# Performance work log

Hardware: AMD Instinct MI355X
Metric: run time of the kernel (lower is better)

## Reference

```python
import jax, jax.numpy as jnp
import numpy as np

B, DIM_Z, N_SAMPLES = 256, 64, 32
LOG_2PI = float(np.log(2.0 * np.pi))
VAR_EPS = 0.0001


def log_pdf(mean, logvar, zs):
    # elementwise Gaussian log-density (per dim), matching torch log_pdf
    return -0.5 * LOG_2PI - 0.5 * logvar - (zs - mean) ** 2 / (2.0 * jnp.exp(logvar) + VAR_EPS)


def setup_inputs() -> dict:
    key = jax.random.key(0)
    k1, k2, k3, k4, k5 = jax.random.split(key, 5)
    return {
        "prior_mean": jax.random.normal(k1, (B, DIM_Z), dtype=jnp.float32),
        "prior_logvar": jax.random.normal(k2, (B, DIM_Z), dtype=jnp.float32),
        "post_mean": jax.random.normal(k3, (B, DIM_Z), dtype=jnp.float32),
        "post_logvar": jax.random.normal(k4, (B, DIM_Z), dtype=jnp.float32),
        "eps": jax.random.normal(k5, (B, DIM_Z, N_SAMPLES), dtype=jnp.float32),
    }


def reference(prior_mean, prior_logvar, post_mean, post_logvar, eps):
    batch_size = post_mean.shape[0]
    # reparameterized samples from each posterior: [B, D, S]
    zs = post_mean[:, :, None] + eps * jnp.exp(0.5 * post_logvar)[:, :, None]
    # log p_prior_j(z_{j,d,s}): [B, D, S]
    logp_priors_zs = log_pdf(prior_mean[:, :, None], prior_logvar[:, :, None], zs)
    # log p_post_i(z_{j,d,s}): [B(i), B(j), D, S] -- the big broadcast intermediate
    logp_posts_zs = log_pdf(post_mean[:, None, :, None], post_logvar[:, None, :, None], zs[None])
    # max-stabilized log-mean-exp over posteriors i == logsumexp - log(B)
    logp_agg_post_zs = jax.scipy.special.logsumexp(logp_posts_zs, axis=0) - jnp.log(
        jnp.asarray(batch_size, dtype=logp_posts_zs.dtype)
    )  # [B(j), D, S]
    density_gaps = logp_agg_post_zs - logp_priors_zs  # [B, D, S]
    kl = density_gaps.mean(axis=0)  # [D, S]
    kl = kl.sum(axis=0).mean(axis=-1)  # scalar
    return kl
```

## Files before the change

### kernel.cpp

```cpp
#include <hip/hip_runtime.h>
#include <math.h>

#define BATCH 256
#define DIMZ  64
#define NSAMP 32
#define JB    32

__global__ __launch_bounds__(256) void lpo_tbl_kernel(
    const float* __restrict__ post_mean,
    const float* __restrict__ post_logvar,
    float* __restrict__ tblA,
    float* __restrict__ tblB,
    float* __restrict__ tblC)
{
    constexpr float LOG_2PI = 1.8378770664093453f;
    constexpr float VAR_EPS = 1e-4f;
    constexpr float LOG2E   = 1.4426950408889634f;

    const int d = blockIdx.x;
    const int i = threadIdx.x;

    const float m   = post_mean[i * DIMZ + d];
    const float lv  = post_logvar[i * DIMZ + d];
    const float den = 2.0f * __expf(lv) + VAR_EPS;
    const float C   = LOG2E / den;
    const float B   = 2.0f * m * C;
    const float A   = LOG2E * (-0.5f * LOG_2PI - 0.5f * lv) - m * m * C;

    tblA[d * BATCH + i] = A;
    tblB[d * BATCH + i] = B;
    tblC[d * BATCH + i] = C;
}

__global__ __launch_bounds__(256) void lpo_kl_kernel(
    const float* __restrict__ prior_mean,
    const float* __restrict__ prior_logvar,
    const float* __restrict__ post_mean,
    const float* __restrict__ post_logvar,
    const float* __restrict__ eps,
    const float* __restrict__ tblA,
    const float* __restrict__ tblB,
    const float* __restrict__ tblC,
    float* __restrict__ out)
{
    constexpr float LOG_2PI = 1.8378770664093453f;
    constexpr float VAR_EPS = 1e-4f;
    constexpr float LN2     = 0.6931471805599453f;
    constexpr float LOG_B   = 5.545177444479562f;

    __shared__ float wred[4];

    const int tid = threadIdx.x;
    const int d   = blockIdx.x & (DIMZ - 1);
    const int j0  = (blockIdx.x >> 6) * JB;
    const int s   = tid & (NSAMP - 1);
    const int jj  = tid >> 5;

    float z[4], nz2[4];
    #pragma unroll
    for (int k = 0; k < 4; ++k) {
        const int j  = j0 + jj + 8 * k;
        const float m  = post_mean[j * DIMZ + d];
        const float lv = post_logvar[j * DIMZ + d];
        z[k]   = m + eps[(j * DIMZ + d) * NSAMP + s] * __expf(0.5f * lv);
        nz2[k] = -(z[k] * z[k]);
    }

    const float* __restrict__ Ap = tblA + d * BATCH;
    const float* __restrict__ Bp = tblB + d * BATCH;
    const float* __restrict__ Cp = tblC + d * BATCH;

    float acc[4][4] = {};
    #pragma unroll 4
    for (int i = 0; i < BATCH; i += 4) {
        const float4 Av = *(const float4*)(Ap + i);
        const float4 Bv = *(const float4*)(Bp + i);
        const float4 Cv = *(const float4*)(Cp + i);
        #pragma unroll
        for (int k = 0; k < 4; ++k) {
            acc[0][k] += __builtin_amdgcn_exp2f(
                __builtin_fmaf(Cv.x, nz2[k], __builtin_fmaf(Bv.x, z[k], Av.x)));
            acc[1][k] += __builtin_amdgcn_exp2f(
                __builtin_fmaf(Cv.y, nz2[k], __builtin_fmaf(Bv.y, z[k], Av.y)));
            acc[2][k] += __builtin_amdgcn_exp2f(
                __builtin_fmaf(Cv.z, nz2[k], __builtin_fmaf(Bv.z, z[k], Av.z)));
            acc[3][k] += __builtin_amdgcn_exp2f(
                __builtin_fmaf(Cv.w, nz2[k], __builtin_fmaf(Bv.w, z[k], Av.w)));
        }
    }

    float contrib = 0.0f;
    #pragma unroll
    for (int k = 0; k < 4; ++k) {
        const int j = j0 + jj + 8 * k;
        const float sum = (acc[0][k] + acc[1][k]) + (acc[2][k] + acc[3][k]);
        const float lse_nat = LN2 * __builtin_amdgcn_logf(sum) - LOG_B;

        const float pm   = prior_mean[j * DIMZ + d];
        const float plv  = prior_logvar[j * DIMZ + d];
        const float pden = 2.0f * __expf(plv) + VAR_EPS;
        const float dz   = z[k] - pm;
        const float logp_prior = -0.5f * LOG_2PI - 0.5f * plv - dz * dz / pden;

        contrib += lse_nat - logp_prior;
    }
    contrib *= 1.0f / (BATCH * NSAMP);

    for (int off = 32; off > 0; off >>= 1)
        contrib += __shfl_down(contrib, off);
    if ((tid & 63) == 0) wred[tid >> 6] = contrib;
    __syncthreads();
    if (tid == 0)
        atomicAdd(out, (wred[0] + wred[1]) + (wred[2] + wred[3]));
}

extern "C" void kernel_launch(void* const* d_in, const int* in_sizes, int n_in,
                              void* d_out, int out_size, void* d_ws, size_t ws_size,
                              hipStream_t stream) {
    const float* prior_mean   = (const float*)d_in[0];
    const float* prior_logvar = (const float*)d_in[1];
    const float* post_mean    = (const float*)d_in[2];
    const float* post_logvar  = (const float*)d_in[3];
    const float* eps          = (const float*)d_in[4];
    float* out = (float*)d_out;

    float* tblA = (float*)d_ws;
    float* tblB = tblA + DIMZ * BATCH;
    float* tblC = tblB + DIMZ * BATCH;

    lpo_tbl_kernel<<<dim3(DIMZ), dim3(BATCH), 0, stream>>>(
        post_mean, post_logvar, tblA, tblB, tblC);

    hipMemsetAsync(out, 0, sizeof(float), stream);

    lpo_kl_kernel<<<dim3((BATCH / JB) * DIMZ), dim3(256), 0, stream>>>(
        prior_mean, prior_logvar, post_mean, post_logvar, eps,
        tblA, tblB, tblC, out);
}
```

Baseline: 86.62 us.

## Halve rows per block, use packed FMA, fold output zeroing into table kernel

Each block now covers 16 j-rows instead of 32, so the grid doubles to 1024 blocks and each thread handles 2 z values instead of 4. The inner loop uses 2-wide vector FMAs that can map to packed FP32 instructions on CDNA. The separate memset launch is dropped and the output is zeroed inside the table kernel. In exchange, every table element is read twice as many times in total and per-thread ILP is lower, while exp2 count per thread is unchanged in ratio.

```diff
diff --git a/kernel.cpp b/kernel.cpp
--- a/kernel.cpp
+++ b/kernel.cpp
@@ -4,14 +4,17 @@
 #define BATCH 256
 #define DIMZ  64
 #define NSAMP 32
-#define JB    32
+#define JB    16
+
+typedef float v2f __attribute__((ext_vector_type(2)));
 
 __global__ __launch_bounds__(256) void lpo_tbl_kernel(
     const float* __restrict__ post_mean,
     const float* __restrict__ post_logvar,
     float* __restrict__ tblA,
     float* __restrict__ tblB,
-    float* __restrict__ tblC)
+    float* __restrict__ tblC,
+    float* __restrict__ out)
 {
     constexpr float LOG_2PI = 1.8378770664093453f;
     constexpr float VAR_EPS = 1e-4f;
@@ -19,6 +22,8 @@
 
     const int d = blockIdx.x;
     const int i = threadIdx.x;
+
+    if (d == 0 && i == 0) *out = 0.0f;
 
     const float m   = post_mean[i * DIMZ + d];
     const float lv  = post_logvar[i * DIMZ + d];
@@ -56,44 +61,55 @@
     const int s   = tid & (NSAMP - 1);
     const int jj  = tid >> 5;
 
-    float z[4], nz2[4];
+    float z[2];
     #pragma unroll
-    for (int k = 0; k < 4; ++k) {
+    for (int k = 0; k < 2; ++k) {
         const int j  = j0 + jj + 8 * k;
         const float m  = post_mean[j * DIMZ + d];
         const float lv = post_logvar[j * DIMZ + d];
-        z[k]   = m + eps[(j * DIMZ + d) * NSAMP + s] * __expf(0.5f * lv);
-        nz2[k] = -(z[k] * z[k]);
+        z[k] = m + eps[(j * DIMZ + d) * NSAMP + s] * __expf(0.5f * lv);
     }
+    const v2f zv  = { z[0], z[1] };
+    const v2f nzv = { -z[0] * z[0], -z[1] * z[1] };
 
     const float* __restrict__ Ap = tblA + d * BATCH;
     const float* __restrict__ Bp = tblB + d * BATCH;
     const float* __restrict__ Cp = tblC + d * BATCH;
 
-    float acc[4][4] = {};
+    v2f acc[4] = { {0.f,0.f}, {0.f,0.f}, {0.f,0.f}, {0.f,0.f} };
     #pragma unroll 4
     for (int i = 0; i < BATCH; i += 4) {
         const float4 Av = *(const float4*)(Ap + i);
         const float4 Bv = *(const float4*)(Bp + i);
         const float4 Cv = *(const float4*)(Cp + i);
-        #pragma unroll
-        for (int k = 0; k < 4; ++k) {
-            acc[0][k] += __builtin_amdgcn_exp2f(
-                __builtin_fmaf(Cv.x, nz2[k], __builtin_fmaf(Bv.x, z[k], Av.x)));
-            acc[1][k] += __builtin_amdgcn_exp2f(
-                __builtin_fmaf(Cv.y, nz2[k], __builtin_fmaf(Bv.y, z[k], Av.y)));
-            acc[2][k] += __builtin_amdgcn_exp2f(
-                __builtin_fmaf(Cv.z, nz2[k], __builtin_fmaf(Bv.z, z[k], Av.z)));
-            acc[3][k] += __builtin_amdgcn_exp2f(
-                __builtin_fmaf(Cv.w, nz2[k], __builtin_fmaf(Bv.w, z[k], Av.w)));
+        {
+            const v2f t = __builtin_elementwise_fma((v2f){Cv.x, Cv.x}, nzv,
+                          __builtin_elementwise_fma((v2f){Bv.x, Bv.x}, zv, (v2f){Av.x, Av.x}));
+            acc[0] += (v2f){ __builtin_amdgcn_exp2f(t.x), __builtin_amdgcn_exp2f(t.y) };
+        }
+        {
+            const v2f t = __builtin_elementwise_fma((v2f){Cv.y, Cv.y}, nzv,
+                          __builtin_elementwise_fma((v2f){Bv.y, Bv.y}, zv, (v2f){Av.y, Av.y}));
+            acc[1] += (v2f){ __builtin_amdgcn_exp2f(t.x), __builtin_amdgcn_exp2f(t.y) };
+        }
+        {
+            const v2f t = __builtin_elementwise_fma((v2f){Cv.z, Cv.z}, nzv,
+                          __builtin_elementwise_fma((v2f){Bv.z, Bv.z}, zv, (v2f){Av.z, Av.z}));
+            acc[2] += (v2f){ __builtin_amdgcn_exp2f(t.x), __builtin_amdgcn_exp2f(t.y) };
+        }
+        {
+            const v2f t = __builtin_elementwise_fma((v2f){Cv.w, Cv.w}, nzv,
+                          __builtin_elementwise_fma((v2f){Bv.w, Bv.w}, zv, (v2f){Av.w, Av.w}));
+            acc[3] += (v2f){ __builtin_amdgcn_exp2f(t.x), __builtin_amdgcn_exp2f(t.y) };
         }
     }
+    const v2f accs = (acc[0] + acc[1]) + (acc[2] + acc[3]);
 
     float contrib = 0.0f;
     #pragma unroll
-    for (int k = 0; k < 4; ++k) {
+    for (int k = 0; k < 2; ++k) {
         const int j = j0 + jj + 8 * k;
-        const float sum = (acc[0][k] + acc[1][k]) + (acc[2][k] + acc[3][k]);
+        const float sum = (k == 0) ? accs.x : accs.y;
         const float lse_nat = LN2 * __builtin_amdgcn_logf(sum) - LOG_B;
 
         const float pm   = prior_mean[j * DIMZ + d];
@@ -129,9 +145,7 @@
     float* tblC = tblB + DIMZ * BATCH;
 
     lpo_tbl_kernel<<<dim3(DIMZ), dim3(BATCH), 0, stream>>>(
-        post_mean, post_logvar, tblA, tblB, tblC);
-
-    hipMemsetAsync(out, 0, sizeof(float), stream);
+        post_mean, post_logvar, tblA, tblB, tblC, out);
 
     lpo_kl_kernel<<<dim3((BATCH / JB) * DIMZ), dim3(256), 0, stream>>>(
         prior_mean, prior_logvar, post_mean, post_logvar, eps,
```

Result: faster. 84.25 us (-2.7%).
